# Optimization experiments

Measured on AMD Instinct MI355X. Metric: run time of the kernel, lower is better.

## Reference

```python
import jax, jax.numpy as jnp
import numpy as np

VOCAB, EMB = 100000, 50
KERNEL_NUM, SIGMA, EXACT_SIGMA = 21, 0.1, 0.001
OUT_LAYERS = [10, 5]


def _kernel_params():
    # Mirrors KNRM._get_kernels_layers
    mus = [1.0]
    bin_size = 2.0 / (KERNEL_NUM - 1)
    mus.append(1 - bin_size / 2)
    for i in range(1, KERNEL_NUM - 1):
        mus.append(mus[i] - bin_size)
    mus = list(reversed(mus))
    sigmas = [SIGMA] * (KERNEL_NUM - 1) + [EXACT_SIGMA]
    return np.array(mus, np.float32), np.array(sigmas, np.float32)

MUS, SIGMAS = _kernel_params()


def setup_inputs() -> dict:
    key = jax.random.key(0)
    ks = jax.random.split(key, 12)
    B, LQ, LD = 2048, 32, 256
    emb = jax.random.normal(ks[0], (VOCAB, EMB), jnp.float32)
    emb = emb.at[0].set(0.0)  # padding_idx=0
    query1 = jax.random.randint(ks[1], (B, LQ), 0, VOCAB)
    doc1 = jax.random.randint(ks[2], (B, LD), 0, VOCAB)
    query2 = jax.random.randint(ks[3], (B, LQ), 0, VOCAB)
    doc2 = jax.random.randint(ks[4], (B, LD), 0, VOCAB)
    def lin(k, fan_in, fan_out):
        bound = 1.0 / np.sqrt(fan_in)
        kw, kb = jax.random.split(k)
        w = jax.random.uniform(kw, (fan_out, fan_in), jnp.float32, -bound, bound)
        b = jax.random.uniform(kb, (fan_out,), jnp.float32, -bound, bound)
        return w, b
    w0, b0 = lin(ks[5], KERNEL_NUM, OUT_LAYERS[0])
    w1, b1 = lin(ks[6], OUT_LAYERS[0], OUT_LAYERS[1])
    w2, b2 = lin(ks[7], OUT_LAYERS[1], 1)
    return dict(emb=emb, w0=w0, b0=b0, w1=w1, b1=b1, w2=w2, b2=b2,
                query1=query1, doc1=doc1, query2=query2, doc2=doc2)


def _matching_matrix(emb, query, doc):
    qe = emb[query]                     # [B, Lq, E]
    de = emb[doc]                       # [B, Ld, E]
    qn = qe / (jnp.linalg.norm(qe, axis=-1, keepdims=True) + 1e-13)
    dn = de / (jnp.linalg.norm(de, axis=-1, keepdims=True) + 1e-13)
    return jnp.einsum('bqe,bde->bqd', qn, dn)  # cosine sim [B, Lq, Ld]


def _apply_kernels(mm):
    # Loop over the fixed 21 kernels (structurally distinct mu/sigma),
    # avoiding a [B,Lq,Ld,21] intermediate, as the original does.
    km = []
    for mu, sg in zip(MUS, SIGMAS):
        k = jnp.exp(-(mm - mu) ** 2 / (2.0 * sg * sg))
        km.append(jnp.log1p(k.sum(axis=-1)).sum(axis=-1))  # [B]
    return jnp.stack(km, axis=1)  # [B, K]


def _mlp(x, w0, b0, w1, b1, w2, b2):
    h = jax.nn.relu(x @ w0.T + b0)
    h = jax.nn.relu(h @ w1.T + b1)
    return h @ w2.T + b2  # [B, 1]


def _predict(emb, w0, b0, w1, b1, w2, b2, query, doc):
    mm = _matching_matrix(emb, query, doc)
    ko = _apply_kernels(mm)
    return _mlp(ko, w0, b0, w1, b1, w2, b2)


def reference(emb, w0, b0, w1, b1, w2, b2, query1, doc1, query2, doc2):
    logits1 = _predict(emb, w0, b0, w1, b1, w2, b2, query1, doc1)
    logits2 = _predict(emb, w0, b0, w1, b1, w2, b2, query2, doc2)
    return jax.nn.sigmoid(logits1 - logits2)  # [B, 1]
```

## Files before the change

kernel.cpp:

```cpp
#include <hip/hip_runtime.h>

#define EMB_N 50
#define KP 64
#define LQ 32
#define LD 256
#define KN 21
#define BATCH 2048

typedef short v8s __attribute__((ext_vector_type(8)));
typedef float v4f __attribute__((ext_vector_type(4)));
typedef float v2f __attribute__((ext_vector_type(2)));

#define PK_ACC(d, b)    asm("v_pk_add_f32 %0, %0, %1" : "+v"(d) : "v"(b))
#define PK_MULA(d, b)   asm("v_pk_mul_f32 %0, %0, %1" : "+v"(d) : "v"(b))

__device__ inline short bf16_rne(float f) {
  unsigned u = __float_as_uint(f);
  unsigned r = u + 0x7fffu + ((u >> 16) & 1u);
  return (short)(r >> 16);
}
__device__ inline float bf16_tof(short h) {
  return __uint_as_float(((unsigned)(unsigned short)h) << 16);
}

__global__ __launch_bounds__(256) void vocab_norm_kernel(
    const float* __restrict__ emb, short* __restrict__ vb,
    short* __restrict__ vlo, int vocab)
{
  int gid = blockIdx.x * 256 + threadIdx.x;
  int r = gid >> 3;
  int c = gid & 7;
  if (r >= vocab) return;
  const float* row = emb + (size_t)r * EMB_N;
  float v[8];
#pragma unroll
  for (int k = 0; k < 8; k++) v[k] = 0.f;
  float ss = 0.f;
  int e0 = c * 8;
  if (c < 6) {
    const float2* p = (const float2*)(row + e0);
#pragma unroll
    for (int k = 0; k < 4; k++) {
      float2 t = p[k];
      v[2*k] = t.x; v[2*k+1] = t.y;
      ss = fmaf(t.x, t.x, ss); ss = fmaf(t.y, t.y, ss);
    }
  } else if (c == 6) {
    float2 t = *(const float2*)(row + 48);
    v[0] = t.x; v[1] = t.y;
    ss = fmaf(t.x, t.x, t.y * t.y);
  }
  ss += __shfl_xor(ss, 1);
  ss += __shfl_xor(ss, 2);
  ss += __shfl_xor(ss, 4);
  float inv = 1.0f / (sqrtf(ss) + 1e-13f);
  short hi[8], lo[8];
#pragma unroll
  for (int k = 0; k < 8; k++) {
    float f = v[k] * inv;
    hi[k] = bf16_rne(f);
    lo[k] = bf16_rne(f - bf16_tof(hi[k]));
  }
  size_t o = (size_t)r * KP + e0;
  *(uint4*)(vb + o)  = *(const uint4*)hi;
  *(uint4*)(vlo + o) = *(const uint4*)lo;
}

__device__ __constant__ const float CJ[KN] = {
  2.5261639e-20f, 2.0469719e-16f, 6.1019363e-13f, 6.6915861e-10f, 2.6995785e-7f,
  4.0065297e-5f,  2.1874911e-3f,  4.3936937e-2f,  0.32465247f,    0.88249690f,
  0.88249690f,    0.32465247f,    4.3936937e-2f,  2.1874911e-3f,  4.0065297e-5f,
  2.6995785e-7f,  6.6915861e-10f, 6.1019363e-13f, 2.0469719e-16f, 2.5261639e-20f,
  1.0f
};

__global__ __launch_bounds__(256, 5) void knrm_main_kernel(
    const short* __restrict__ vb, const short* __restrict__ vlo,
    const int* __restrict__ q1, const int* __restrict__ d1,
    const int* __restrict__ q2, const int* __restrict__ d2,
    const float* __restrict__ w0, const float* __restrict__ b0,
    const float* __restrict__ w1, const float* __restrict__ b1,
    const float* __restrict__ w2, const float* __restrict__ b2,
    float* __restrict__ lgbuf)
{
  __shared__ float part[4][16][KN];
  __shared__ float Sqex[LQ];
  __shared__ float ko[KN];
  __shared__ float h0s[10];
  __shared__ float h1s[5];

  const int pair = blockIdx.x >> 11;
  const int b = blockIdx.x & (BATCH - 1);
  const int tid = threadIdx.x;
  const int wave = tid >> 6;
  const int lane = tid & 63;
  const int l15 = lane & 15;
  const int quad = lane >> 4;
  const int qtile = wave >> 1;
  const int thalf = wave & 1;

  const int* qp = pair ? q2 : q1;
  const int* dp = pair ? d2 : d1;

  if (tid < LQ) Sqex[tid] = 0.f;

  int qtok = qp[b * LQ + qtile * 16 + l15];
  const short* qh = vb  + (size_t)qtok * KP + quad * 8;
  const short* ql = vlo + (size_t)qtok * KP + quad * 8;
  v8s Bh0 = *(const v8s*)(qh);
  v8s Bh1 = *(const v8s*)(qh + 32);
  v8s Bl0 = *(const v8s*)(ql);
  v8s Bl1 = *(const v8s*)(ql + 32);

  int mydtok = dp[b * LD + tid];
  int dtoks[8];
#pragma unroll
  for (int t = 0; t < 8; t++)
    dtoks[t] = dp[b * LD + (thalf * 8 + t) * 16 + l15];

  __syncthreads();

#pragma unroll
  for (int qq = 0; qq < LQ; qq++) {
    int qt = qp[b * LQ + qq];
    unsigned long long m = __ballot(mydtok == qt && qt != 0);
    if (lane == 0 && m)
      atomicAdd(&Sqex[qq], (float)__popcll(m));
  }

  v2f U2[10];
#pragma unroll
  for (int i = 0; i < 10; i++) U2[i] = (v2f){0.f, 0.f};

  const short* dptr0 = vb + (size_t)dtoks[0] * KP + quad * 8;
  v8s A0 = *(const v8s*)(dptr0);
  v8s A1 = *(const v8s*)(dptr0 + 32);

#pragma unroll 2
  for (int t = 0; t < 8; t++) {
    v8s N0, N1;
    if (t < 7) {
      const short* dptr = vb + (size_t)dtoks[t + 1] * KP + quad * 8;
      N0 = *(const v8s*)(dptr);
      N1 = *(const v8s*)(dptr + 32);
    }
    v4f C = {0.f, 0.f, 0.f, 0.f};
    C = __builtin_amdgcn_mfma_f32_16x16x32_bf16(A0, Bh0, C, 0, 0, 0);
    C = __builtin_amdgcn_mfma_f32_16x16x32_bf16(A1, Bh1, C, 0, 0, 0);
    C = __builtin_amdgcn_mfma_f32_16x16x32_bf16(A0, Bl0, C, 0, 0, 0);
    C = __builtin_amdgcn_mfma_f32_16x16x32_bf16(A1, Bl1, C, 0, 0, 0);
#pragma unroll
    for (int r = 0; r < 4; r++) {
      float x = C[r];
      float gc = __builtin_amdgcn_exp2f(x * fmaf(-72.1347520f, x, 7.2134752f));
      float ex = 14.4269504f * x;
      float rr1 = __builtin_amdgcn_exp2f(ex);
      float ri  = __builtin_amdgcn_exp2f(-ex);
      v2f p  = {gc, gc * ri};
      v2f rr = {rr1, ri};
#pragma unroll
      for (int k2 = 0; k2 < 10; k2++) {
        PK_ACC(U2[k2], p);
        PK_MULA(p, rr);
      }
    }
    if (t < 7) { A0 = N0; A1 = N1; }
  }

#pragma unroll
  for (int i = 0; i < 10; i++) {
    float ux = U2[i].x, uy = U2[i].y;
    ux += __shfl_xor(ux, 16);  uy += __shfl_xor(uy, 16);
    ux += __shfl_xor(ux, 32);  uy += __shfl_xor(uy, 32);
    if (quad == 0) {
      part[wave][l15][10 + i] = ux;
      part[wave][l15][9 - i]  = uy;
    }
  }
  __syncthreads();

  {
    int qq = tid & 31;
    int qi = qq & 15, qt2 = qq >> 4;
    int jb = tid >> 5;
#pragma unroll
    for (int k = 0; k < 3; k++) {
      int j = jb + 8 * k;
      float l = 0.f;
      if (j < KN) {
        float s = (j < 20) ? part[qt2 * 2][qi][j] + part[qt2 * 2 + 1][qi][j]
                           : Sqex[qq];
        float y = fmaf(CJ[j], s, 1.0f);
        l = 0.69314718f * __builtin_amdgcn_logf(y);
      }
      l += __shfl_xor(l, 1);  l += __shfl_xor(l, 2);
      l += __shfl_xor(l, 4);  l += __shfl_xor(l, 8);
      l += __shfl_xor(l, 16);
      if (qq == 0 && j < KN) ko[j] = l;
    }
  }
  __syncthreads();

  if (tid < 10) {
    float h = b0[tid];
#pragma unroll
    for (int k = 0; k < KN; k++) h = fmaf(w0[tid * KN + k], ko[k], h);
    h0s[tid] = fmaxf(h, 0.f);
  }
  __syncthreads();
  if (tid < 5) {
    float h = b1[tid];
#pragma unroll
    for (int k = 0; k < 10; k++) h = fmaf(w1[tid * 10 + k], h0s[k], h);
    h1s[tid] = fmaxf(h, 0.f);
  }
  __syncthreads();
  if (tid == 0) {
    float h = b2[0];
#pragma unroll
    for (int k = 0; k < 5; k++) h = fmaf(w2[k], h1s[k], h);
    lgbuf[pair * BATCH + b] = h;
  }
}

__global__ __launch_bounds__(256) void knrm_combine_kernel(
    const float* __restrict__ lgbuf, float* __restrict__ out)
{
  int i = blockIdx.x * 256 + threadIdx.x;
  if (i < BATCH) {
    float z = lgbuf[i] - lgbuf[BATCH + i];
    out[i] = 1.0f / (1.0f + expf(-z));
  }
}

extern "C" void kernel_launch(void* const* d_in, const int* in_sizes, int n_in,
                              void* d_out, int out_size, void* d_ws, size_t ws_size,
                              hipStream_t stream)
{
  const float* emb = (const float*)d_in[0];
  const float* w0  = (const float*)d_in[1];
  const float* b0  = (const float*)d_in[2];
  const float* w1  = (const float*)d_in[3];
  const float* b1  = (const float*)d_in[4];
  const float* w2  = (const float*)d_in[5];
  const float* b2  = (const float*)d_in[6];
  const int* q1 = (const int*)d_in[7];
  const int* dd1 = (const int*)d_in[8];
  const int* q2 = (const int*)d_in[9];
  const int* dd2 = (const int*)d_in[10];
  float* out = (float*)d_out;

  int vocab = in_sizes[0] / EMB_N;
  int B = in_sizes[7] / LQ;

  float* lgbuf = (float*)d_ws;
  short* vb  = (short*)(lgbuf + 2 * BATCH);
  short* vlo = vb + (size_t)vocab * KP;

  vocab_norm_kernel<<<(vocab * 8 + 255) / 256, 256, 0, stream>>>(emb, vb, vlo, vocab);
  knrm_main_kernel<<<2 * B, 256, 0, stream>>>(vb, vlo, q1, dd1, q2, dd2,
                                              w0, b0, w1, b1, w2, b2, lgbuf);
  knrm_combine_kernel<<<(B + 255) / 256, 256, 0, stream>>>(lgbuf, out);
}
```

Baseline: 142.3 us.

## Raise occupancy target, drop doc-token prefetch, interleave two exp-chains in kernel loop

Raises the launch-bounds minimum blocks per CU from 5 to 6 and stops preloading the eight document token ids and the next tile's embeddings into registers. Each iteration now loads its token and embedding rows just in time, with the loop no longer unrolled. The kernel evaluation now interleaves two independent geometric-series chains so the packed add/mul dependencies overlap. The aim is higher occupancy and more instruction-level parallelism to hide latency, at the cost of losing the software prefetch, which exposes gather latency inside each iteration.

```diff
diff --git a/kernel.cpp b/kernel.cpp
--- a/kernel.cpp
+++ b/kernel.cpp
@@ -74,7 +74,7 @@
   1.0f
 };
 
-__global__ __launch_bounds__(256, 5) void knrm_main_kernel(
+__global__ __launch_bounds__(256, 6) void knrm_main_kernel(
     const short* __restrict__ vb, const short* __restrict__ vlo,
     const int* __restrict__ q1, const int* __restrict__ d1,
     const int* __restrict__ q2, const int* __restrict__ d2,
@@ -113,10 +113,6 @@
   v8s Bl1 = *(const v8s*)(ql + 32);
 
   int mydtok = dp[b * LD + tid];
-  int dtoks[8];
-#pragma unroll
-  for (int t = 0; t < 8; t++)
-    dtoks[t] = dp[b * LD + (thalf * 8 + t) * 16 + l15];
 
   __syncthreads();
 
@@ -132,39 +128,46 @@
 #pragma unroll
   for (int i = 0; i < 10; i++) U2[i] = (v2f){0.f, 0.f};
 
-  const short* dptr0 = vb + (size_t)dtoks[0] * KP + quad * 8;
-  v8s A0 = *(const v8s*)(dptr0);
-  v8s A1 = *(const v8s*)(dptr0 + 32);
-
-#pragma unroll 2
+#pragma unroll 1
   for (int t = 0; t < 8; t++) {
-    v8s N0, N1;
-    if (t < 7) {
-      const short* dptr = vb + (size_t)dtoks[t + 1] * KP + quad * 8;
-      N0 = *(const v8s*)(dptr);
-      N1 = *(const v8s*)(dptr + 32);
-    }
+    int dtok = dp[b * LD + (thalf * 8 + t) * 16 + l15];
+    const short* dptr = vb + (size_t)dtok * KP + quad * 8;
+    v8s A0 = *(const v8s*)(dptr);
+    v8s A1 = *(const v8s*)(dptr + 32);
+
     v4f C = {0.f, 0.f, 0.f, 0.f};
     C = __builtin_amdgcn_mfma_f32_16x16x32_bf16(A0, Bh0, C, 0, 0, 0);
     C = __builtin_amdgcn_mfma_f32_16x16x32_bf16(A1, Bh1, C, 0, 0, 0);
     C = __builtin_amdgcn_mfma_f32_16x16x32_bf16(A0, Bl0, C, 0, 0, 0);
     C = __builtin_amdgcn_mfma_f32_16x16x32_bf16(A1, Bl1, C, 0, 0, 0);
-#pragma unroll
-    for (int r = 0; r < 4; r++) {
-      float x = C[r];
-      float gc = __builtin_amdgcn_exp2f(x * fmaf(-72.1347520f, x, 7.2134752f));
-      float ex = 14.4269504f * x;
-      float rr1 = __builtin_amdgcn_exp2f(ex);
-      float ri  = __builtin_amdgcn_exp2f(-ex);
-      v2f p  = {gc, gc * ri};
-      v2f rr = {rr1, ri};
+
+#pragma unroll
+    for (int rp = 0; rp < 2; rp++) {
+      v2f p0, p1, rr0, rr1;
+      {
+        float x = C[rp * 2];
+        float gc = __builtin_amdgcn_exp2f(x * fmaf(-72.1347520f, x, 7.2134752f));
+        float ex = 14.4269504f * x;
+        float e1 = __builtin_amdgcn_exp2f(ex);
+        float ei = __builtin_amdgcn_exp2f(-ex);
+        p0 = (v2f){gc, gc * ei};  rr0 = (v2f){e1, ei};
+      }
+      {
+        float x = C[rp * 2 + 1];
+        float gc = __builtin_amdgcn_exp2f(x * fmaf(-72.1347520f, x, 7.2134752f));
+        float ex = 14.4269504f * x;
+        float e1 = __builtin_amdgcn_exp2f(ex);
+        float ei = __builtin_amdgcn_exp2f(-ex);
+        p1 = (v2f){gc, gc * ei};  rr1 = (v2f){e1, ei};
+      }
 #pragma unroll
       for (int k2 = 0; k2 < 10; k2++) {
-        PK_ACC(U2[k2], p);
-        PK_MULA(p, rr);
-      }
-    }
-    if (t < 7) { A0 = N0; A1 = N1; }
+        PK_ACC(U2[k2], p0);
+        PK_MULA(p0, rr0);
+        PK_ACC(U2[k2], p1);
+        PK_MULA(p1, rr1);
+      }
+    }
   }
 
 #pragma unroll
```

Result: no change. 143.9 us (+1.1%).
